# Optimization experiments

Measured on AMD Instinct MI355X. Metric: run time of the kernel, lower is better.

## Reference

```python
import jax, jax.numpy as jnp
import numpy as np

NPOINT, RADIUS, NSAMPLE = 2048, 0.2, 32
BN_EPS = 1e-5


def _fps(xyz, npoint):
    # Farthest point sampling. xyz: [B,N,3] -> idx [B,npoint] (int32).
    B, N, _ = xyz.shape
    def step(carry, _):
        dist, farthest = carry  # dist [B,N], farthest [B]
        centroid = xyz[jnp.arange(B), farthest]            # [B,3]
        d = jnp.sum((xyz - centroid[:, None, :]) ** 2, -1)  # [B,N]
        dist = jnp.minimum(dist, d)
        nxt = jnp.argmax(dist, axis=-1).astype(jnp.int32)
        return (dist, nxt), farthest
    init = (jnp.full((B, N), 1e10, xyz.dtype), jnp.zeros((B,), jnp.int32))
    _, idxs = jax.lax.scan(step, init, None, length=npoint)
    return jnp.transpose(idxs)  # [B, npoint]


def _ball_query(radius, nsample, xyz, new_xyz):
    # xyz [B,N,3], new_xyz [B,S,3] -> idx [B,S,nsample]
    B, N, _ = xyz.shape
    sqr = jnp.sum((new_xyz[:, :, None, :] - xyz[:, None, :, :]) ** 2, -1)  # [B,S,N]
    ar = jnp.arange(N, dtype=jnp.int32)[None, None, :]
    idx = jnp.where(sqr > radius * radius, N, ar)
    idx = jnp.sort(idx, axis=-1)[..., :nsample]
    first = idx[..., :1]
    return jnp.where(idx == N, first, idx)


def _index_points(points, idx):
    # points [B,N,C], idx [B,...] -> [B,...,C]
    B = points.shape[0]
    bidx = jnp.arange(B).reshape((B,) + (1,) * (idx.ndim - 1))
    return points[bidx, idx]


def _mlp_layer(x, w, b, g, bt):
    # 1x1 Conv2d over [B,S,K,Cin] + inference BatchNorm (mean=0, var=1) + ReLU
    z = jnp.einsum('bskc,oc->bsko', x, w) + b
    z = g * (z / jnp.sqrt(1.0 + BN_EPS)) + bt
    return jax.nn.relu(z)


def setup_inputs():
    key = jax.random.key(0)
    ks = jax.random.split(key, 8)
    B, N, C = 8, 8192, 64
    inp = {
        'xyz': jax.random.uniform(ks[0], (B, N, 3), jnp.float32),
        'feats': jax.random.normal(ks[1], (B, N, C), jnp.float32),
    }
    dims = [C + 3, 64, 64, 128]
    for i in range(3):
        cin, cout = dims[i], dims[i + 1]
        inp[f'w{i+1}'] = jax.random.normal(ks[2 + i], (cout, cin), jnp.float32) / np.float32(np.sqrt(cin))
        inp[f'b{i+1}'] = jnp.zeros((cout,), jnp.float32)
        inp[f'g{i+1}'] = jnp.ones((cout,), jnp.float32)
        inp[f'bt{i+1}'] = jnp.zeros((cout,), jnp.float32)
    return inp


def reference(xyz, feats, w1, b1, g1, bt1, w2, b2, g2, bt2, w3, b3, g3, bt3):
    center_idx = _fps(xyz, NPOINT)                 # [B,S]
    new_xyz = _index_points(xyz, center_idx)       # [B,S,3]
    idx = _ball_query(RADIUS, NSAMPLE, xyz, new_xyz)  # [B,S,K]
    grouped_xyz = _index_points(xyz, idx)          # [B,S,K,3]
    grouped_dp = (grouped_xyz - new_xyz[:, :, None, :]) / RADIUS  # normalize_dp
    grouped_feats = _index_points(feats, idx)      # [B,S,K,C]
    grouped = jnp.concatenate([grouped_dp, grouped_feats], axis=-1)  # [B,S,K,C+3]
    x = _mlp_layer(grouped, w1, b1, g1, bt1)
    x = _mlp_layer(x, w2, b2, g2, bt2)
    x = _mlp_layer(x, w3, b3, g3, bt3)
    new_feats = jnp.max(x, axis=2)                 # max over neighbors -> [B,S,Cout]
    return new_xyz, new_feats
```

## Files before the change

### kernel.cpp

```cpp
#include <hip/hip_runtime.h>
#include <cstdint>

typedef unsigned short u16;
typedef _Float16 f16x8  __attribute__((ext_vector_type(8)));
typedef float    f32x4  __attribute__((ext_vector_type(4)));
typedef float    v2f    __attribute__((ext_vector_type(2)));

#define DEV static __device__ __forceinline__

constexpr int kB = 8;
constexpr int kN = 8192;
constexpr int kS = 2048;
constexpr int kK = 32;
constexpr int kC = 64;

DEV v2f vmin2(v2f a, v2f b){ v2f r; r.x = fminf(a.x,b.x); r.y = fminf(a.y,b.y); return r; }

template<int CTRL>
DEV float dppmax(float v){
  int x = __builtin_amdgcn_mov_dpp(__builtin_bit_cast(int, v), CTRL, 0xF, 0xF, true);
  float o = __builtin_bit_cast(float, x);
  return fmaxf(v, o);
}
DEV float readlanef(float v, int l){
  return __builtin_bit_cast(float, __builtin_amdgcn_readlane(__builtin_bit_cast(int, v), l));
}

__global__ __launch_bounds__(256) void prep_kernel(const float* __restrict__ xyz,
                                                   float* __restrict__ X,
                                                   float* __restrict__ Y,
                                                   float* __restrict__ Z){
  int i = blockIdx.x * 256 + threadIdx.x;
  if (i < kB * kN){
    X[i] = xyz[i*3+0];
    Y[i] = xyz[i*3+1];
    Z[i] = xyz[i*3+2];
  }
}

__global__ __launch_bounds__(512) __attribute__((amdgpu_waves_per_eu(2, 2)))
void fps_kernel(const float* __restrict__ X,
                const float* __restrict__ Y,
                const float* __restrict__ Z,
                int* __restrict__ cidx,
                float* __restrict__ oxyz){
  __shared__ __align__(16) float lx[kN];
  __shared__ __align__(16) float ly[kN];
  __shared__ __align__(16) float lz[kN];
  __shared__ __align__(16) int   cl_i[kS];
  __shared__ __align__(16) float cl_c[kS*3];
  __shared__ uint64_t sk[2][8];
  const int b    = blockIdx.x;
  const int tid  = threadIdx.x;
  const int lane = tid & 63;
  const int wid  = tid >> 6;
  const float* xb = X + b*kN;
  const float* yb = Y + b*kN;
  const float* zb = Z + b*kN;

  v2f px[8], py[8], pz[8], dd[8];
  const int p0 = tid*16;
  {
    f32x4 t0 = *(const f32x4*)(xb+p0);   f32x4 t1 = *(const f32x4*)(xb+p0+4);
    f32x4 t2 = *(const f32x4*)(xb+p0+8); f32x4 t3 = *(const f32x4*)(xb+p0+12);
    *(f32x4*)(lx+p0)=t0; *(f32x4*)(lx+p0+4)=t1; *(f32x4*)(lx+p0+8)=t2; *(f32x4*)(lx+p0+12)=t3;
    px[0]=(v2f){t0.x,t0.y}; px[1]=(v2f){t0.z,t0.w}; px[2]=(v2f){t1.x,t1.y}; px[3]=(v2f){t1.z,t1.w};
    px[4]=(v2f){t2.x,t2.y}; px[5]=(v2f){t2.z,t2.w}; px[6]=(v2f){t3.x,t3.y}; px[7]=(v2f){t3.z,t3.w};
  }
  {
    f32x4 t0 = *(const f32x4*)(yb+p0);   f32x4 t1 = *(const f32x4*)(yb+p0+4);
    f32x4 t2 = *(const f32x4*)(yb+p0+8); f32x4 t3 = *(const f32x4*)(yb+p0+12);
    *(f32x4*)(ly+p0)=t0; *(f32x4*)(ly+p0+4)=t1; *(f32x4*)(ly+p0+8)=t2; *(f32x4*)(ly+p0+12)=t3;
    py[0]=(v2f){t0.x,t0.y}; py[1]=(v2f){t0.z,t0.w}; py[2]=(v2f){t1.x,t1.y}; py[3]=(v2f){t1.z,t1.w};
    py[4]=(v2f){t2.x,t2.y}; py[5]=(v2f){t2.z,t2.w}; py[6]=(v2f){t3.x,t3.y}; py[7]=(v2f){t3.z,t3.w};
  }
  {
    f32x4 t0 = *(const f32x4*)(zb+p0);   f32x4 t1 = *(const f32x4*)(zb+p0+4);
    f32x4 t2 = *(const f32x4*)(zb+p0+8); f32x4 t3 = *(const f32x4*)(zb+p0+12);
    *(f32x4*)(lz+p0)=t0; *(f32x4*)(lz+p0+4)=t1; *(f32x4*)(lz+p0+8)=t2; *(f32x4*)(lz+p0+12)=t3;
    pz[0]=(v2f){t0.x,t0.y}; pz[1]=(v2f){t0.z,t0.w}; pz[2]=(v2f){t1.x,t1.y}; pz[3]=(v2f){t1.z,t1.w};
    pz[4]=(v2f){t2.x,t2.y}; pz[5]=(v2f){t2.z,t2.w}; pz[6]=(v2f){t3.x,t3.y}; pz[7]=(v2f){t3.z,t3.w};
  }
  #pragma unroll
  for (int j = 0; j < 8; j++){ dd[j].x = 1e10f; dd[j].y = 1e10f; }

  __syncthreads();
  float cx = lx[0], cy = ly[0], cz = lz[0];
  if (tid == 0){
    cl_i[0] = 0;
    cl_c[0] = cx; cl_c[1] = cy; cl_c[2] = cz;
  }

  #pragma unroll 1
  for (int t = 1; t < kS; t++){
    float q[8];
    {
      #pragma clang fp contract(off)
      v2f c2x; c2x.x = cx; c2x.y = cx;
      v2f c2y; c2y.x = cy; c2y.y = cy;
      v2f c2z; c2z.x = cz; c2z.y = cz;
      #pragma unroll
      for (int j = 0; j < 8; j++){
        v2f dx = px[j] - c2x;
        v2f dy = py[j] - c2y;
        v2f dz = pz[j] - c2z;
        v2f d  = dx*dx + dy*dy;
        d = d + dz*dz;
        dd[j] = vmin2(dd[j], d);
        q[j]  = fmaxf(dd[j].x, dd[j].y);
      }
    }
    float lmax = fmaxf(fmaxf(q[0], q[1]), q[2]);
    lmax = fmaxf(fmaxf(lmax, q[3]), q[4]);
    lmax = fmaxf(fmaxf(lmax, q[5]), q[6]);
    lmax = fmaxf(lmax, q[7]);
    int sl = 0;
    #pragma unroll
    for (int j = 7; j >= 0; j--){
      if (dd[j].y == lmax) sl = 2*j + 1;
      if (dd[j].x == lmax) sl = 2*j;
    }
    float r = lmax;
    r = dppmax<0xB1>(r);
    r = dppmax<0x4E>(r);
    r = dppmax<0x114>(r);
    r = dppmax<0x118>(r);
    r = dppmax<0x142>(r);
    r = dppmax<0x143>(r);
    float wmax = readlanef(r, 63);
    unsigned long long mk = __ballot(lmax == wmax);
    int wl   = (int)__builtin_ctzll(mk);
    int widx = __builtin_amdgcn_readlane(tid*16 + sl, wl);
    if (lane == 0)
      sk[t & 1][wid] = ((uint64_t)__builtin_bit_cast(uint32_t, wmax) << 32)
                     | (uint32_t)widx;
    __syncthreads();
    uint64_t kk = sk[t & 1][lane & 7];
    float m8 = __builtin_bit_cast(float, (uint32_t)(kk >> 32));
    int   i8 = (int)(uint32_t)kk;
    float sx = lx[i8], sy = ly[i8], sz = lz[i8];
    float r2 = m8;
    r2 = dppmax<0xB1>(r2);
    r2 = dppmax<0x4E>(r2);
    r2 = dppmax<0x114>(r2);
    float bmax = readlanef(r2, 7);
    unsigned long long mk2 = __ballot(m8 == bmax);
    int ww = (int)__builtin_ctzll(mk2);
    int w  = __builtin_amdgcn_readlane(i8, ww);
    cx = readlanef(sx, ww); cy = readlanef(sy, ww); cz = readlanef(sz, ww);
    if (tid == 0){
      cl_i[t] = w;
      cl_c[3*t+0] = cx; cl_c[3*t+1] = cy; cl_c[3*t+2] = cz;
    }
  }

  __syncthreads();
  #pragma unroll
  for (int i = 0; i < kS/512; i++){
    int s = i*512 + tid;
    cidx[b*kS + s] = cl_i[s];
  }
  #pragma unroll
  for (int i = 0; i < (kS*3)/512; i++){
    int s = i*512 + tid;
    oxyz[(size_t)b*kS*3 + s] = cl_c[s];
  }
}

__global__ __launch_bounds__(256) void ballq_kernel(const float* __restrict__ X,
                                                    const float* __restrict__ Y,
                                                    const float* __restrict__ Z,
                                                    const int* __restrict__ cidx,
                                                    u16* __restrict__ bidx){
  const int lw   = threadIdx.x >> 6;
  const int lane = threadIdx.x & 63;
  const int wv   = blockIdx.x * 4 + lw;
  __shared__ u16 buf[4][kK];
  const int b = wv >> 11;
  const float* xb = X + b*kN;
  const float* yb = Y + b*kN;
  const float* zb = Z + b*kN;
  const int ci = cidx[wv];
  const float ccx = xb[ci], ccy = yb[ci], ccz = zb[ci];
  const float R2 = (float)(0.2*0.2);

  int cnt = 0;
  for (int base = 0; base < kN; base += 64){
    float sq;
    {
      #pragma clang fp contract(off)
      int p = base + lane;
      float dx = xb[p] - ccx;
      float dy = yb[p] - ccy;
      float dz = zb[p] - ccz;
      sq = dx*dx + dy*dy;
      sq = sq + dz*dz;
    }
    bool in = !(sq > R2);
    unsigned long long mk = __ballot(in);
    int pos = cnt + __popcll(mk & ((1ull << lane) - 1ull));
    if (in && pos < kK) buf[lw][pos] = (u16)(base + lane);
    cnt += (int)__popcll(mk);
    if (cnt >= kK) break;
  }
  u16 first = buf[lw][0];
  if (lane < kK){
    int c = cnt < kK ? cnt : kK;
    bidx[(size_t)wv*kK + lane] = (lane < c) ? buf[lw][lane] : first;
  }
}

DEV f16x8 ld8cvt(const float* p){
  f32x4 a = *(const f32x4*)p;
  f32x4 b = *(const f32x4*)(p + 4);
  f16x8 h;
  #pragma unroll
  for (int j = 0; j < 4; j++){ h[j] = (_Float16)a[j]; h[4+j] = (_Float16)b[j]; }
  return h;
}

__global__ __launch_bounds__(256) void mlp_kernel(
    const float* __restrict__ feats,
    const float* __restrict__ w1, const float* __restrict__ b1, const float* __restrict__ g1, const float* __restrict__ bt1,
    const float* __restrict__ w2, const float* __restrict__ b2, const float* __restrict__ g2, const float* __restrict__ bt2,
    const float* __restrict__ w3, const float* __restrict__ b3, const float* __restrict__ g3, const float* __restrict__ bt3,
    const float* __restrict__ X, const float* __restrict__ Y, const float* __restrict__ Z,
    const int* __restrict__ cidx, const u16* __restrict__ bidx,
    float* __restrict__ ofeat)
{
  constexpr int HP = 72;
  __shared__ _Float16 H[4][32*HP];
  const int lw   = threadIdx.x >> 6;
  const int lane = threadIdx.x & 63;
  const int nl   = lane & 15;
  const int kg   = lane >> 4;
  const int gw   = blockIdx.x * 4 + lw;
  const float INVS = 0.99999500003749968f;

  f16x8 wf1[4][3];
  #pragma unroll
  for (int nt = 0; nt < 4; nt++){
    #pragma unroll
    for (int kt = 0; kt < 3; kt++){
      f16x8 h;
      #pragma unroll
      for (int j = 0; j < 8; j++){
        int k = kt*32 + kg*8 + j;
        int c = (k < 64) ? (k + 3) : ((k < 67) ? (k - 64) : -1);
        h[j] = (c >= 0) ? (_Float16)w1[(nt*16 + nl)*67 + c] : (_Float16)0.0f;
      }
      wf1[nt][kt] = h;
    }
  }
  f16x8 wf2[4][2];
  #pragma unroll
  for (int nt = 0; nt < 4; nt++)
    #pragma unroll
    for (int kt = 0; kt < 2; kt++)
      wf2[nt][kt] = ld8cvt(w2 + (nt*16 + nl)*64 + kt*32 + kg*8);
  f16x8 wf3[8][2];
  #pragma unroll
  for (int nt = 0; nt < 8; nt++)
    #pragma unroll
    for (int kt = 0; kt < 2; kt++)
      wf3[nt][kt] = ld8cvt(w3 + (nt*16 + nl)*64 + kt*32 + kg*8);

  float a1c[4], e1c[4], a2c[4], e2c[4], a3c[8], e3c[8];
  #pragma unroll
  for (int nt = 0; nt < 4; nt++){
    int c = nt*16 + nl;
    a1c[nt] = g1[c] * INVS; e1c[nt] = fmaf(a1c[nt], b1[c], bt1[c]);
    a2c[nt] = g2[c] * INVS; e2c[nt] = fmaf(a2c[nt], b2[c], bt2[c]);
  }
  #pragma unroll
  for (int nt = 0; nt < 8; nt++){
    int c = nt*16 + nl;
    a3c[nt] = g3[c] * INVS; e3c[nt] = fmaf(a3c[nt], b3[c], bt3[c]);
  }

  _Float16* Hw = &H[lw][0];
  const f32x4 z4 = {0.f, 0.f, 0.f, 0.f};

  #pragma unroll 1
  for (int i = 0; i < 8; i++){
    const int cid = gw*8 + i;
    const int b   = cid >> 11;
    const float* fb = feats + (size_t)b * kN * kC;

    int my = (int)bidx[(size_t)cid*kK + (lane & 31)];
    int n0 = __shfl(my, nl);
    int n1 = __shfl(my, 16 + nl);
    f16x8 a00 = ld8cvt(fb + (size_t)n0*kC +      kg*8);
    f16x8 a01 = ld8cvt(fb + (size_t)n0*kC + 32 + kg*8);
    f16x8 a10 = ld8cvt(fb + (size_t)n1*kC +      kg*8);
    f16x8 a11 = ld8cvt(fb + (size_t)n1*kC + 32 + kg*8);
    const float* xb = X + b*kN; const float* yb = Y + b*kN; const float* zb = Z + b*kN;
    int ci = cidx[cid];
    float ccx = xb[ci], ccy = yb[ci], ccz = zb[ci];
    float dpx = (xb[my] - ccx) / 0.2f;
    float dpy = (yb[my] - ccy) / 0.2f;
    float dpz = (zb[my] - ccz) / 0.2f;
    float x0 = __shfl(dpx, nl),      y0 = __shfl(dpy, nl),      zz0 = __shfl(dpz, nl);
    float x1 = __shfl(dpx, 16 + nl), y1 = __shfl(dpy, 16 + nl), zz1 = __shfl(dpz, 16 + nl);
    f16x8 ad0 = {0,0,0,0,0,0,0,0}, ad1 = {0,0,0,0,0,0,0,0};
    if (kg == 0){
      ad0[0] = (_Float16)x0; ad0[1] = (_Float16)y0; ad0[2] = (_Float16)zz0;
      ad1[0] = (_Float16)x1; ad1[1] = (_Float16)y1; ad1[2] = (_Float16)zz1;
    }

    f32x4 c1[2][4];
    #pragma unroll
    for (int nt = 0; nt < 4; nt++){
      f32x4 acc = z4;
      acc = __builtin_amdgcn_mfma_f32_16x16x32_f16(ad0, wf1[nt][2], acc, 0, 0, 0);
      acc = __builtin_amdgcn_mfma_f32_16x16x32_f16(a00, wf1[nt][0], acc, 0, 0, 0);
      acc = __builtin_amdgcn_mfma_f32_16x16x32_f16(a01, wf1[nt][1], acc, 0, 0, 0);
      c1[0][nt] = acc;
      acc = z4;
      acc = __builtin_amdgcn_mfma_f32_16x16x32_f16(ad1, wf1[nt][2], acc, 0, 0, 0);
      acc = __builtin_amdgcn_mfma_f32_16x16x32_f16(a10, wf1[nt][0], acc, 0, 0, 0);
      acc = __builtin_amdgcn_mfma_f32_16x16x32_f16(a11, wf1[nt][1], acc, 0, 0, 0);
      c1[1][nt] = acc;
    }
    #pragma unroll
    for (int mt = 0; mt < 2; mt++)
      #pragma unroll
      for (int nt = 0; nt < 4; nt++)
        #pragma unroll
        for (int r = 0; r < 4; r++){
          float h = fmaxf(fmaf(a1c[nt], c1[mt][nt][r], e1c[nt]), 0.f);
          Hw[(mt*16 + kg*4 + r)*HP + nt*16 + nl] = (_Float16)h;
        }
    f16x8 h1[2][2];
    #pragma unroll
    for (int mt = 0; mt < 2; mt++)
      #pragma unroll
      for (int kt = 0; kt < 2; kt++)
        h1[mt][kt] = *(const f16x8*)(Hw + (mt*16 + nl)*HP + kt*32 + kg*8);
    f32x4 c2[2][4];
    #pragma unroll
    for (int mt = 0; mt < 2; mt++)
      #pragma unroll
      for (int nt = 0; nt < 4; nt++){
        f32x4 acc = z4;
        acc = __builtin_amdgcn_mfma_f32_16x16x32_f16(h1[mt][0], wf2[nt][0], acc, 0, 0, 0);
        acc = __builtin_amdgcn_mfma_f32_16x16x32_f16(h1[mt][1], wf2[nt][1], acc, 0, 0, 0);
        c2[mt][nt] = acc;
      }
    #pragma unroll
    for (int mt = 0; mt < 2; mt++)
      #pragma unroll
      for (int nt = 0; nt < 4; nt++)
        #pragma unroll
        for (int r = 0; r < 4; r++){
          float h = fmaxf(fmaf(a2c[nt], c2[mt][nt][r], e2c[nt]), 0.f);
          Hw[(mt*16 + kg*4 + r)*HP + nt*16 + nl] = (_Float16)h;
        }
    f16x8 h2[2][2];
    #pragma unroll
    for (int mt = 0; mt < 2; mt++)
      #pragma unroll
      for (int kt = 0; kt < 2; kt++)
        h2[mt][kt] = *(const f16x8*)(Hw + (mt*16 + nl)*HP + kt*32 + kg*8);
    #pragma unroll
    for (int nt = 0; nt < 8; nt++){
      f32x4 d0 = z4, d1 = z4;
      d0 = __builtin_amdgcn_mfma_f32_16x16x32_f16(h2[0][0], wf3[nt][0], d0, 0, 0, 0);
      d0 = __builtin_amdgcn_mfma_f32_16x16x32_f16(h2[0][1], wf3[nt][1], d0, 0, 0, 0);
      d1 = __builtin_amdgcn_mfma_f32_16x16x32_f16(h2[1][0], wf3[nt][0], d1, 0, 0, 0);
      d1 = __builtin_amdgcn_mfma_f32_16x16x32_f16(h2[1][1], wf3[nt][1], d1, 0, 0, 0);
      float m = -1e30f;
      #pragma unroll
      for (int r = 0; r < 4; r++){
        m = fmaxf(m, fmaf(a3c[nt], d0[r], e3c[nt]));
        m = fmaxf(m, fmaf(a3c[nt], d1[r], e3c[nt]));
      }
      m = fmaxf(m, 0.f);
      m = fmaxf(m, __shfl_xor(m, 16));
      m = fmaxf(m, __shfl_xor(m, 32));
      if (lane < 16) ofeat[(size_t)cid*128 + nt*16 + nl] = m;
    }
  }
}

extern "C" void kernel_launch(void* const* d_in, const int* in_sizes, int n_in,
                              void* d_out, int out_size, void* d_ws, size_t ws_size,
                              hipStream_t stream){
  (void)in_sizes; (void)n_in; (void)out_size; (void)ws_size;
  const float* xyz   = (const float*)d_in[0];
  const float* feats = (const float*)d_in[1];
  const float* w1  = (const float*)d_in[2];
  const float* b1  = (const float*)d_in[3];
  const float* g1  = (const float*)d_in[4];
  const float* bt1 = (const float*)d_in[5];
  const float* w2  = (const float*)d_in[6];
  const float* b2  = (const float*)d_in[7];
  const float* g2  = (const float*)d_in[8];
  const float* bt2 = (const float*)d_in[9];
  const float* w3  = (const float*)d_in[10];
  const float* b3  = (const float*)d_in[11];
  const float* g3  = (const float*)d_in[12];
  const float* bt3 = (const float*)d_in[13];
  float* out = (float*)d_out;

  float* X  = (float*)d_ws;
  float* Y  = X + kB*kN;
  float* Z  = Y + kB*kN;
  int*   ci = (int*)(Z + kB*kN);
  u16*   bi = (u16*)(ci + kB*kS);

  hipLaunchKernelGGL(prep_kernel,  dim3(256),  dim3(256), 0, stream, xyz, X, Y, Z);
  hipLaunchKernelGGL(fps_kernel,   dim3(kB),   dim3(512), 0, stream, X, Y, Z, ci, out);
  hipLaunchKernelGGL(ballq_kernel, dim3(4096), dim3(256), 0, stream, X, Y, Z, ci, bi);
  hipLaunchKernelGGL(mlp_kernel,   dim3(512),  dim3(256), 0, stream,
                     feats, w1, b1, g1, bt1, w2, b2, g2, bt2, w3, b3, g3, bt3,
                     X, Y, Z, ci, bi, out + (size_t)kB*kS*3);
}
```

Before: 1.889 ms.

## Halve FPS block to 4 waves with 32 points per thread

The farthest-point-sampling kernel now runs 256 threads per batch instead of 512, and each thread holds 32 points in registers instead of 16. The cross-wave reduction drops from 8 to 4 partial results. The per-thread max becomes a packed vector max tree, and the new centroid is read from LDS by index instead of being broadcast through readlane. This cuts barrier and cross-wave reduction cost in the 2047-step serial loop, but doubles the per-thread ALU work each step and uses more registers per thread.

Result: no change. 1.882 ms, median of 2 (-0.4%).

```diff
diff --git a/kernel.cpp b/kernel.cpp
--- a/kernel.cpp
+++ b/kernel.cpp
@@ -15,6 +15,7 @@
 constexpr int kC = 64;
 
 DEV v2f vmin2(v2f a, v2f b){ v2f r; r.x = fminf(a.x,b.x); r.y = fminf(a.y,b.y); return r; }
+DEV v2f vmax2(v2f a, v2f b){ v2f r; r.x = fmaxf(a.x,b.x); r.y = fmaxf(a.y,b.y); return r; }
 
 template<int CTRL>
 DEV float dppmax(float v){
@@ -38,7 +39,7 @@
   }
 }
 
-__global__ __launch_bounds__(512) __attribute__((amdgpu_waves_per_eu(2, 2)))
+__global__ __launch_bounds__(256) __attribute__((amdgpu_waves_per_eu(1, 1)))
 void fps_kernel(const float* __restrict__ X,
                 const float* __restrict__ Y,
                 const float* __restrict__ Z,
@@ -49,7 +50,7 @@
   __shared__ __align__(16) float lz[kN];
   __shared__ __align__(16) int   cl_i[kS];
   __shared__ __align__(16) float cl_c[kS*3];
-  __shared__ uint64_t sk[2][8];
+  __shared__ uint64_t sk[2][4];
   const int b    = blockIdx.x;
   const int tid  = threadIdx.x;
   const int lane = tid & 63;
@@ -58,31 +59,34 @@
   const float* yb = Y + b*kN;
   const float* zb = Z + b*kN;
 
-  v2f px[8], py[8], pz[8], dd[8];
-  const int p0 = tid*16;
-  {
-    f32x4 t0 = *(const f32x4*)(xb+p0);   f32x4 t1 = *(const f32x4*)(xb+p0+4);
-    f32x4 t2 = *(const f32x4*)(xb+p0+8); f32x4 t3 = *(const f32x4*)(xb+p0+12);
-    *(f32x4*)(lx+p0)=t0; *(f32x4*)(lx+p0+4)=t1; *(f32x4*)(lx+p0+8)=t2; *(f32x4*)(lx+p0+12)=t3;
-    px[0]=(v2f){t0.x,t0.y}; px[1]=(v2f){t0.z,t0.w}; px[2]=(v2f){t1.x,t1.y}; px[3]=(v2f){t1.z,t1.w};
-    px[4]=(v2f){t2.x,t2.y}; px[5]=(v2f){t2.z,t2.w}; px[6]=(v2f){t3.x,t3.y}; px[7]=(v2f){t3.z,t3.w};
-  }
-  {
-    f32x4 t0 = *(const f32x4*)(yb+p0);   f32x4 t1 = *(const f32x4*)(yb+p0+4);
-    f32x4 t2 = *(const f32x4*)(yb+p0+8); f32x4 t3 = *(const f32x4*)(yb+p0+12);
-    *(f32x4*)(ly+p0)=t0; *(f32x4*)(ly+p0+4)=t1; *(f32x4*)(ly+p0+8)=t2; *(f32x4*)(ly+p0+12)=t3;
-    py[0]=(v2f){t0.x,t0.y}; py[1]=(v2f){t0.z,t0.w}; py[2]=(v2f){t1.x,t1.y}; py[3]=(v2f){t1.z,t1.w};
-    py[4]=(v2f){t2.x,t2.y}; py[5]=(v2f){t2.z,t2.w}; py[6]=(v2f){t3.x,t3.y}; py[7]=(v2f){t3.z,t3.w};
-  }
-  {
-    f32x4 t0 = *(const f32x4*)(zb+p0);   f32x4 t1 = *(const f32x4*)(zb+p0+4);
-    f32x4 t2 = *(const f32x4*)(zb+p0+8); f32x4 t3 = *(const f32x4*)(zb+p0+12);
-    *(f32x4*)(lz+p0)=t0; *(f32x4*)(lz+p0+4)=t1; *(f32x4*)(lz+p0+8)=t2; *(f32x4*)(lz+p0+12)=t3;
-    pz[0]=(v2f){t0.x,t0.y}; pz[1]=(v2f){t0.z,t0.w}; pz[2]=(v2f){t1.x,t1.y}; pz[3]=(v2f){t1.z,t1.w};
-    pz[4]=(v2f){t2.x,t2.y}; pz[5]=(v2f){t2.z,t2.w}; pz[6]=(v2f){t3.x,t3.y}; pz[7]=(v2f){t3.z,t3.w};
-  }
-  #pragma unroll
-  for (int j = 0; j < 8; j++){ dd[j].x = 1e10f; dd[j].y = 1e10f; }
+  v2f px[16], py[16], pz[16], dd[16];
+  const int p0 = tid*32;
+  #pragma unroll
+  for (int g = 0; g < 4; g++){
+    f32x4 t0 = *(const f32x4*)(xb+p0+g*8);
+    f32x4 t1 = *(const f32x4*)(xb+p0+g*8+4);
+    *(f32x4*)(lx+p0+g*8)=t0; *(f32x4*)(lx+p0+g*8+4)=t1;
+    px[4*g+0]=(v2f){t0.x,t0.y}; px[4*g+1]=(v2f){t0.z,t0.w};
+    px[4*g+2]=(v2f){t1.x,t1.y}; px[4*g+3]=(v2f){t1.z,t1.w};
+  }
+  #pragma unroll
+  for (int g = 0; g < 4; g++){
+    f32x4 t0 = *(const f32x4*)(yb+p0+g*8);
+    f32x4 t1 = *(const f32x4*)(yb+p0+g*8+4);
+    *(f32x4*)(ly+p0+g*8)=t0; *(f32x4*)(ly+p0+g*8+4)=t1;
+    py[4*g+0]=(v2f){t0.x,t0.y}; py[4*g+1]=(v2f){t0.z,t0.w};
+    py[4*g+2]=(v2f){t1.x,t1.y}; py[4*g+3]=(v2f){t1.z,t1.w};
+  }
+  #pragma unroll
+  for (int g = 0; g < 4; g++){
+    f32x4 t0 = *(const f32x4*)(zb+p0+g*8);
+    f32x4 t1 = *(const f32x4*)(zb+p0+g*8+4);
+    *(f32x4*)(lz+p0+g*8)=t0; *(f32x4*)(lz+p0+g*8+4)=t1;
+    pz[4*g+0]=(v2f){t0.x,t0.y}; pz[4*g+1]=(v2f){t0.z,t0.w};
+    pz[4*g+2]=(v2f){t1.x,t1.y}; pz[4*g+3]=(v2f){t1.z,t1.w};
+  }
+  #pragma unroll
+  for (int j = 0; j < 16; j++){ dd[j].x = 1e10f; dd[j].y = 1e10f; }
 
   __syncthreads();
   float cx = lx[0], cy = ly[0], cz = lz[0];
@@ -93,30 +97,30 @@
 
   #pragma unroll 1
   for (int t = 1; t < kS; t++){
-    float q[8];
     {
       #pragma clang fp contract(off)
       v2f c2x; c2x.x = cx; c2x.y = cx;
       v2f c2y; c2y.x = cy; c2y.y = cy;
       v2f c2z; c2z.x = cz; c2z.y = cz;
       #pragma unroll
-      for (int j = 0; j < 8; j++){
+      for (int j = 0; j < 16; j++){
         v2f dx = px[j] - c2x;
         v2f dy = py[j] - c2y;
         v2f dz = pz[j] - c2z;
         v2f d  = dx*dx + dy*dy;
         d = d + dz*dz;
         dd[j] = vmin2(dd[j], d);
-        q[j]  = fmaxf(dd[j].x, dd[j].y);
       }
     }
-    float lmax = fmaxf(fmaxf(q[0], q[1]), q[2]);
-    lmax = fmaxf(fmaxf(lmax, q[3]), q[4]);
-    lmax = fmaxf(fmaxf(lmax, q[5]), q[6]);
-    lmax = fmaxf(lmax, q[7]);
+    v2f m0 = vmax2(vmax2(dd[0],  dd[1]),  vmax2(dd[2],  dd[3]));
+    v2f m1 = vmax2(vmax2(dd[4],  dd[5]),  vmax2(dd[6],  dd[7]));
+    v2f m2 = vmax2(vmax2(dd[8],  dd[9]),  vmax2(dd[10], dd[11]));
+    v2f m3 = vmax2(vmax2(dd[12], dd[13]), vmax2(dd[14], dd[15]));
+    v2f mm = vmax2(vmax2(m0, m1), vmax2(m2, m3));
+    float lmax = fmaxf(mm.x, mm.y);
     int sl = 0;
     #pragma unroll
-    for (int j = 7; j >= 0; j--){
+    for (int j = 15; j >= 0; j--){
       if (dd[j].y == lmax) sl = 2*j + 1;
       if (dd[j].x == lmax) sl = 2*j;
     }
@@ -130,24 +134,21 @@
     float wmax = readlanef(r, 63);
     unsigned long long mk = __ballot(lmax == wmax);
     int wl   = (int)__builtin_ctzll(mk);
-    int widx = __builtin_amdgcn_readlane(tid*16 + sl, wl);
+    int widx = __builtin_amdgcn_readlane(tid*32 + sl, wl);
     if (lane == 0)
       sk[t & 1][wid] = ((uint64_t)__builtin_bit_cast(uint32_t, wmax) << 32)
                      | (uint32_t)widx;
     __syncthreads();
-    uint64_t kk = sk[t & 1][lane & 7];
-    float m8 = __builtin_bit_cast(float, (uint32_t)(kk >> 32));
-    int   i8 = (int)(uint32_t)kk;
-    float sx = lx[i8], sy = ly[i8], sz = lz[i8];
-    float r2 = m8;
+    uint64_t kk = sk[t & 1][lane & 3];
+    float m4 = __builtin_bit_cast(float, (uint32_t)(kk >> 32));
+    int   i4 = (int)(uint32_t)kk;
+    float r2 = m4;
     r2 = dppmax<0xB1>(r2);
     r2 = dppmax<0x4E>(r2);
-    r2 = dppmax<0x114>(r2);
-    float bmax = readlanef(r2, 7);
-    unsigned long long mk2 = __ballot(m8 == bmax);
+    unsigned long long mk2 = __ballot(m4 == r2);
     int ww = (int)__builtin_ctzll(mk2);
-    int w  = __builtin_amdgcn_readlane(i8, ww);
-    cx = readlanef(sx, ww); cy = readlanef(sy, ww); cz = readlanef(sz, ww);
+    int w  = __builtin_amdgcn_readlane(i4, ww);
+    cx = lx[w]; cy = ly[w]; cz = lz[w];
     if (tid == 0){
       cl_i[t] = w;
       cl_c[3*t+0] = cx; cl_c[3*t+1] = cy; cl_c[3*t+2] = cz;
@@ -156,13 +157,13 @@
 
   __syncthreads();
   #pragma unroll
-  for (int i = 0; i < kS/512; i++){
-    int s = i*512 + tid;
+  for (int i = 0; i < kS/256; i++){
+    int s = i*256 + tid;
     cidx[b*kS + s] = cl_i[s];
   }
   #pragma unroll
-  for (int i = 0; i < (kS*3)/512; i++){
-    int s = i*512 + tid;
+  for (int i = 0; i < (kS*3)/256; i++){
+    int s = i*256 + tid;
     oxyz[(size_t)b*kS*3 + s] = cl_c[s];
   }
 }
@@ -410,7 +411,7 @@
   u16*   bi = (u16*)(ci + kB*kS);
 
   hipLaunchKernelGGL(prep_kernel,  dim3(256),  dim3(256), 0, stream, xyz, X, Y, Z);
-  hipLaunchKernelGGL(fps_kernel,   dim3(kB),   dim3(512), 0, stream, X, Y, Z, ci, out);
+  hipLaunchKernelGGL(fps_kernel,   dim3(kB),   dim3(256), 0, stream, X, Y, Z, ci, out);
   hipLaunchKernelGGL(ballq_kernel, dim3(4096), dim3(256), 0, stream, X, Y, Z, ci, bi);
   hipLaunchKernelGGL(mlp_kernel,   dim3(512),  dim3(256), 0, stream,
                      feats, w1, b1, g1, bt1, w2, b2, g2, bt2, w3, b3, g3, bt3,
```
